# Performance work log

Hardware: AMD Instinct MI355X
Metric: run time of the kernel (lower is better)

Reference implementation:

```python
import jax, jax.numpy as jnp
import numpy as np

B, H, S, D = 4, 16, 2048, 64


def setup_inputs() -> dict:
    key = jax.random.key(0)
    kq, kk, kv, kp = jax.random.split(key, 4)
    query = jax.random.normal(kq, (B, H, S, D), dtype=jnp.float32)
    k = jax.random.normal(kk, (B, H, S, D), dtype=jnp.float32)
    value = jax.random.normal(kv, (B, H, S, D), dtype=jnp.float32)
    # 0/1 key-padding mask, broadcastable against the [S, S] causal mask
    padding_mask = jax.random.randint(kp, (B, 1, 1, S), 0, 2, dtype=jnp.int32)
    return {"query": query, "key": k, "value": value, "padding_mask": padding_mask}


def reference(query, key, value, padding_mask):
    d_k = query.shape[-1]
    seq_len = query.shape[-2]
    # scores: [B, H, S, S]
    scores = jnp.einsum("bhqd,bhkd->bhqk", query, key) / jnp.sqrt(jnp.float32(d_k))
    # causal mask: 1 above diagonal
    future = jnp.triu(jnp.ones((seq_len, seq_len), dtype=jnp.float32), k=1)
    combined = future + padding_mask.astype(jnp.float32)  # values in {0,1,2}
    # faithful to torch masked_fill(combined_mask == 1, -1e9): only exact 1 is masked
    scores = jnp.where(combined == 1.0, jnp.float32(-1e9), scores)
    attention_weights = jax.nn.softmax(scores, axis=-1)
    result = attention_weights @ value  # [B, H, S, D]
    return result, attention_weights
```

## Files before the change

### kernel.cpp

```cpp
#include <hip/hip_runtime.h>

#define SEQ 2048
#define DH  64
#define NH  16
#define NB  4
#define NHEADS (NB * NH)
#define NKT 32
#define QT  32
#define NQT (SEQ / QT)
#define NBLK (NHEADS * NQT)
#define KTILE_SH 8192
#define QTILE_SH 4096

typedef _Float16 f16x8 __attribute__((ext_vector_type(8)));
typedef _Float16 f16x4 __attribute__((ext_vector_type(4)));
typedef short    s16x8 __attribute__((ext_vector_type(8)));
typedef float    f32x4 __attribute__((ext_vector_type(4)));

#define MF32(a,b,c) __builtin_amdgcn_mfma_f32_16x16x32_f16(a,b,c,0,0,0)
#define MF16(a,b,c) __builtin_amdgcn_mfma_f32_16x16x16f16(a,b,c,0,0,0)

static __device__ __forceinline__ short f16b(float x) {
    _Float16 h = (_Float16)x;
    return __builtin_bit_cast(short, h);
}

__global__ __launch_bounds__(256) void prep(
    const float* __restrict__ Q, const float* __restrict__ K,
    const float* __restrict__ V, const int* __restrict__ pad,
    short* __restrict__ qimg, short* __restrict__ kimg,
    short* __restrict__ vimg, unsigned* __restrict__ pm)
{
    const int t    = threadIdx.x;
    const int kt   = blockIdx.x & (NKT - 1);
    const int head = blockIdx.x >> 5;
    const size_t rowbase = ((size_t)head * SEQ + (size_t)kt * 64) * DH;

    {
        const int row = t >> 2;
        const int c0  = (t & 3) * 16;
        const int lj  = row & 15;

        {
            const float4* gp = (const float4*)(K + rowbase + (size_t)row * DH + c0);
            const float4 v0 = gp[0], v1 = gp[1], v2 = gp[2], v3 = gp[3];
            const float x[16] = {v0.x,v0.y,v0.z,v0.w, v1.x,v1.y,v1.z,v1.w,
                                 v2.x,v2.y,v2.z,v2.w, v3.x,v3.y,v3.z,v3.w};
            short* tb = kimg + ((size_t)head * NKT + kt) * KTILE_SH + (row >> 4) * 2048;
#pragma unroll
            for (int cg = 0; cg < 2; ++cg) {
                const int col0 = c0 + cg * 8;
                const int dh = col0 >> 5, lg = (col0 & 31) >> 3;
                s16x8 hi8, lo8;
#pragma unroll
                for (int j = 0; j < 8; ++j) {
                    const float xv = x[cg * 8 + j];
                    _Float16 h = (_Float16)xv;
                    hi8[j] = __builtin_bit_cast(short, h);
                    lo8[j] = f16b(xv - (float)h);
                }
                *(s16x8*)&tb[dh * 1024 +       (lg * 16 + lj) * 8] = hi8;
                *(s16x8*)&tb[dh * 1024 + 512 + (lg * 16 + lj) * 8] = lo8;
            }
        }
        {
            const float4* gp = (const float4*)(Q + rowbase + (size_t)row * DH + c0);
            const float4 v0 = gp[0], v1 = gp[1], v2 = gp[2], v3 = gp[3];
            const float x[16] = {v0.x,v0.y,v0.z,v0.w, v1.x,v1.y,v1.z,v1.w,
                                 v2.x,v2.y,v2.z,v2.w, v3.x,v3.y,v3.z,v3.w};
            const int qtile = kt * 2 + (row >> 5);
            const int m     = (row >> 4) & 1;
            short* tb = qimg + ((size_t)head * NQT + qtile) * QTILE_SH + m * 2048;
#pragma unroll
            for (int cg = 0; cg < 2; ++cg) {
                const int col0 = c0 + cg * 8;
                const int dh = col0 >> 5, lg = (col0 & 31) >> 3;
                s16x8 hi8, lo8;
#pragma unroll
                for (int j = 0; j < 8; ++j) {
                    const float xv = x[cg * 8 + j];
                    _Float16 h = (_Float16)xv;
                    hi8[j] = __builtin_bit_cast(short, h);
                    lo8[j] = f16b(xv - (float)h);
                }
                *(s16x8*)&tb[dh * 1024 +       (lg * 16 + lj) * 8] = hi8;
                *(s16x8*)&tb[dh * 1024 + 512 + (lg * 16 + lj) * 8] = lo8;
            }
        }
    }
    {
        const int kc = t >> 6, l = t & 63;
        const int lg = l >> 4, lj = l & 15;
        short* tb = vimg + ((size_t)head * NKT + kt) * KTILE_SH + kc * 2048;
#pragma unroll
        for (int dt = 0; dt < 4; ++dt) {
            s16x8 o;
#pragma unroll
            for (int j = 0; j < 4; ++j) {
                const float xv = V[rowbase + (size_t)(kc * 16 + lg * 4 + j) * DH + dt * 16 + lj];
                _Float16 h = (_Float16)xv;
                o[j]     = __builtin_bit_cast(short, h);
                o[4 + j] = f16b(xv - (float)h);
            }
            *(s16x8*)&tb[dt * 512 + l * 8] = o;
        }
    }
    if (blockIdx.x == 0) {
        const int b = t >> 6, klc = t & 63;
        unsigned mword = 0;
#pragma unroll
        for (int kt2 = 0; kt2 < NKT; ++kt2)
            mword |= (unsigned)(pad[b * SEQ + kt2 * 64 + klc] & 1) << kt2;
        pm[t] = mword;
    }
}

struct KF { f16x8 h0, l0, h1, l1; };

#define LDKF(dst_, kt_) do {                                                   \
    const short* p_ = kb + (size_t)(kt_) * KTILE_SH;                           \
    dst_.h0 = *(const f16x8*)(p_ +        l * 8);                              \
    dst_.l0 = *(const f16x8*)(p_ +  512 + l * 8);                              \
    dst_.h1 = *(const f16x8*)(p_ + 1024 + l * 8);                              \
    dst_.l1 = *(const f16x8*)(p_ + 1536 + l * 8);                              \
} while (0)

#define QK12(kf_, a0_, a1_) do {                                               \
    a0_ = MF32(kf_.h0, qh[0][0], a0_);  a1_ = MF32(kf_.h0, qh[1][0], a1_);     \
    a0_ = MF32(kf_.h0, ql[0][0], a0_);  a1_ = MF32(kf_.h0, ql[1][0], a1_);     \
    a0_ = MF32(kf_.l0, qh[0][0], a0_);  a1_ = MF32(kf_.l0, qh[1][0], a1_);     \
    a0_ = MF32(kf_.h1, qh[0][1], a0_);  a1_ = MF32(kf_.h1, qh[1][1], a1_);     \
    a0_ = MF32(kf_.h1, ql[0][1], a0_);  a1_ = MF32(kf_.h1, ql[1][1], a1_);     \
    a0_ = MF32(kf_.l1, qh[0][1], a0_);  a1_ = MF32(kf_.l1, qh[1][1], a1_);     \
} while (0)

#define P1BODY(kt_, kf_) do {                                                  \
    const short* vp_ = vb + (size_t)(kt_) * KTILE_SH;                          \
    f16x8 vfs_[4];                                                             \
    _Pragma("unroll") for (int dt = 0; dt < 4; ++dt)                           \
        vfs_[dt] = *(const f16x8*)(vp_ + dt * 512 + l * 8);                    \
    f32x4 a0_ = (f32x4){0.f,0.f,0.f,0.f}, a1_ = (f32x4){0.f,0.f,0.f,0.f};      \
    QK12(kf_, a0_, a1_);                                                       \
    const int kab_ = (kt_) * 64 + wk * 16 + lg * 4;                            \
    f16x4 w16_[2];                                                             \
    _Pragma("unroll") for (int m = 0; m < 2; ++m) {                            \
        const f32x4 av_ = m ? a1_ : a0_;                                       \
        const int qg_ = qglob + m * 16;                                        \
        float e_[4];                                                           \
        _Pragma("unroll") for (int r = 0; r < 4; ++r) {                        \
            const int ka_ = kab_ + r;                                          \
            const int pd_ = (int)((pmq[r] >> (kt_)) & 1u);                     \
            const bool msk_ = ((ka_ > qg_) != (pd_ == 1));                     \
            e_[r] = __expf((msk_ ? -8.0e9f : av_[r]) * 0.125f);                \
        }                                                                      \
        rs[m] += (e_[0] + e_[1]) + (e_[2] + e_[3]);                            \
        w16_[m] = (f16x4){(_Float16)e_[0], (_Float16)e_[1],                    \
                          (_Float16)e_[2], (_Float16)e_[3]};                   \
    }                                                                          \
    _Pragma("unroll") for (int dt = 0; dt < 4; ++dt) {                         \
        const f16x4 vh_ = __builtin_shufflevector(vfs_[dt], vfs_[dt], 0,1,2,3);\
        const f16x4 vl_ = __builtin_shufflevector(vfs_[dt], vfs_[dt], 4,5,6,7);\
        ov[0][dt] = MF16(w16_[0], vh_, ov[0][dt]);                             \
        ov[1][dt] = MF16(w16_[1], vh_, ov[1][dt]);                             \
        ov[0][dt] = MF16(w16_[0], vl_, ov[0][dt]);                             \
        ov[1][dt] = MF16(w16_[1], vl_, ov[1][dt]);                             \
    }                                                                          \
} while (0)

#define P2BODY(kt_, kf_) do {                                                  \
    f32x4 a0_ = (f32x4){0.f,0.f,0.f,0.f}, a1_ = (f32x4){0.f,0.f,0.f,0.f};      \
    QK12(kf_, a0_, a1_);                                                       \
    const int kab_ = (kt_) * 64 + wk * 16 + lg * 4;                            \
    _Pragma("unroll") for (int m = 0; m < 2; ++m) {                            \
        const f32x4 av_ = m ? a1_ : a0_;                                       \
        const int qg_ = qglob + m * 16;                                        \
        float e_[4];                                                           \
        _Pragma("unroll") for (int r = 0; r < 4; ++r) {                        \
            const int ka_ = kab_ + r;                                          \
            const int pd_ = (int)((pmq[r] >> (kt_)) & 1u);                     \
            const bool msk_ = ((ka_ > qg_) != (pd_ == 1));                     \
            e_[r] = __expf((msk_ ? -8.0e9f : av_[r]) * 0.125f);                \
        }                                                                      \
        f32x4 w4_;                                                             \
        w4_[0] = e_[0] * invr[m]; w4_[1] = e_[1] * invr[m];                    \
        w4_[2] = e_[2] * invr[m]; w4_[3] = e_[3] * invr[m];                    \
        __builtin_nontemporal_store(w4_, (f32x4*)&out_w[wbm[m] + kab_]);       \
    }                                                                          \
} while (0)

__global__ __launch_bounds__(256, 3) void attn_fwd(
    const short* __restrict__ QI, const short* __restrict__ KI,
    const short* __restrict__ VI, const unsigned* __restrict__ PM,
    float* __restrict__ out_res, float* __restrict__ out_w)
{
    __shared__ float s_op[4][QT][65];
    __shared__ float s_red[QT][4];

    const int t = threadIdx.x;
    int bid = blockIdx.x;
    bid = (bid & 7) * (NBLK / 8) + (bid >> 3);

    const int qtile = bid & (NQT - 1);
    const int head  = bid >> 6;
    const int q0    = qtile * QT;
    const size_t hoff = (size_t)head * SEQ * DH;
    const size_t woff = (size_t)head * SEQ * SEQ;

    const int l  = t & 63;
    const int wk = t >> 6;
    const int lj = l & 15;
    const int lg = l >> 4;
    const int qglob = q0 + lj;

    const short* kb  = KI + (size_t)head * NKT * KTILE_SH + wk * 2048;
    const short* vb  = VI + (size_t)head * NKT * KTILE_SH + wk * 2048;
    const short* qbp = QI + ((size_t)head * NQT + qtile) * QTILE_SH;

    f16x8 qh[2][2], ql[2][2];
#pragma unroll
    for (int m = 0; m < 2; ++m)
#pragma unroll
        for (int dh = 0; dh < 2; ++dh) {
            qh[m][dh] = *(const f16x8*)(qbp + m * 2048 + dh * 1024 +       l * 8);
            ql[m][dh] = *(const f16x8*)(qbp + m * 2048 + dh * 1024 + 512 + l * 8);
        }

    int pmq[4];
#pragma unroll
    for (int r = 0; r < 4; ++r)
        pmq[r] = PM[(head >> 4) * 64 + wk * 16 + lg * 4 + r];

    float rs[2] = {0.f, 0.f};
    f32x4 ov[2][4];
#pragma unroll
    for (int m = 0; m < 2; ++m)
#pragma unroll
        for (int dt = 0; dt < 4; ++dt) ov[m][dt] = (f32x4){0.f,0.f,0.f,0.f};

    KF kfA, kfB;
    LDKF(kfA, 0);
#pragma unroll 1
    for (int it = 0; it < NKT / 2; ++it) {
        const int kt0 = it * 2, kt1 = kt0 + 1;
        LDKF(kfB, kt1);
        P1BODY(kt0, kfA);
        LDKF(kfA, (kt1 + 1) & (NKT - 1));
        P1BODY(kt1, kfB);
    }

#pragma unroll
    for (int m = 0; m < 2; ++m) {
        float v = rs[m];
        v += __shfl_xor(v, 16, 64);
        v += __shfl_xor(v, 32, 64);
        rs[m] = v;
    }
    if (lg == 0) {
        s_red[lj][wk]      = rs[0];
        s_red[16 + lj][wk] = rs[1];
    }
#pragma unroll
    for (int m = 0; m < 2; ++m)
#pragma unroll
        for (int dt = 0; dt < 4; ++dt)
#pragma unroll
            for (int r = 0; r < 4; ++r)
                s_op[wk][m * 16 + lg * 4 + r][dt * 16 + lj] = ov[m][dt][r];
    __syncthreads();

    {
        const int q  = t >> 3;
        const int c0 = (t & 7) * 8;
        const float inv = 1.0f / (s_red[q][0] + s_red[q][1] + s_red[q][2] + s_red[q][3]);
        float4 o0, o1;
        o0.x = (s_op[0][q][c0+0]+s_op[1][q][c0+0]+s_op[2][q][c0+0]+s_op[3][q][c0+0]) * inv;
        o0.y = (s_op[0][q][c0+1]+s_op[1][q][c0+1]+s_op[2][q][c0+1]+s_op[3][q][c0+1]) * inv;
        o0.z = (s_op[0][q][c0+2]+s_op[1][q][c0+2]+s_op[2][q][c0+2]+s_op[3][q][c0+2]) * inv;
        o0.w = (s_op[0][q][c0+3]+s_op[1][q][c0+3]+s_op[2][q][c0+3]+s_op[3][q][c0+3]) * inv;
        o1.x = (s_op[0][q][c0+4]+s_op[1][q][c0+4]+s_op[2][q][c0+4]+s_op[3][q][c0+4]) * inv;
        o1.y = (s_op[0][q][c0+5]+s_op[1][q][c0+5]+s_op[2][q][c0+5]+s_op[3][q][c0+5]) * inv;
        o1.z = (s_op[0][q][c0+6]+s_op[1][q][c0+6]+s_op[2][q][c0+6]+s_op[3][q][c0+6]) * inv;
        o1.w = (s_op[0][q][c0+7]+s_op[1][q][c0+7]+s_op[2][q][c0+7]+s_op[3][q][c0+7]) * inv;
        float* op = out_res + hoff + (size_t)(q0 + q) * DH + c0;
        *(float4*)op       = o0;
        *(float4*)(op + 4) = o1;
    }

    float invr[2];
    invr[0] = 1.0f / (s_red[lj][0]      + s_red[lj][1]      + s_red[lj][2]      + s_red[lj][3]);
    invr[1] = 1.0f / (s_red[16 + lj][0] + s_red[16 + lj][1] + s_red[16 + lj][2] + s_red[16 + lj][3]);
    size_t wbm[2];
    wbm[0] = woff + (size_t)(q0 + lj) * SEQ;
    wbm[1] = woff + (size_t)(q0 + 16 + lj) * SEQ;

    LDKF(kfA, 0);
#pragma unroll 1
    for (int it = 0; it < NKT / 2; ++it) {
        const int kt0 = it * 2, kt1 = kt0 + 1;
        LDKF(kfB, kt1);
        P2BODY(kt0, kfA);
        LDKF(kfA, (kt1 + 1) & (NKT - 1));
        P2BODY(kt1, kfB);
    }
}

extern "C" void kernel_launch(void* const* d_in, const int* in_sizes, int n_in,
                              void* d_out, int out_size, void* d_ws, size_t ws_size,
                              hipStream_t stream) {
    const float* Q   = (const float*)d_in[0];
    const float* K   = (const float*)d_in[1];
    const float* V   = (const float*)d_in[2];
    const int*   pad = (const int*)d_in[3];
    float* out_res = (float*)d_out;
    float* out_w   = out_res + (size_t)NB * NH * SEQ * DH;

    short* qimg = (short*)d_ws;
    short* kimg = qimg + (size_t)NHEADS * NQT * QTILE_SH;
    short* vimg = kimg + (size_t)NHEADS * NKT * KTILE_SH;
    unsigned* pm = (unsigned*)(vimg + (size_t)NHEADS * NKT * KTILE_SH);

    prep<<<dim3(NHEADS * NKT), 256, 0, stream>>>(Q, K, V, pad, qimg, kimg, vimg, pm);
    attn_fwd<<<dim3(NBLK), 256, 0, stream>>>(qimg, kimg, vimg, pm, out_res, out_w);
}
```

Baseline: 1.362 ms.

## Double query tile per block to 64 rows and prefetch V fragments

Each block now covers 64 query rows instead of 32. Every K/V fragment loaded from global/L2 is therefore reused across four 16-row MFMA groups instead of two, which halves the K and V traffic per query. V fragments are also double-buffered alongside K so their loads overlap the previous tile's compute. The cost is higher register use (more Q fragments and accumulators), so launch bounds drop to 2 blocks per CU and occupancy may fall.

```diff
diff --git a/kernel.cpp b/kernel.cpp
--- a/kernel.cpp
+++ b/kernel.cpp
@@ -6,11 +6,11 @@
 #define NB  4
 #define NHEADS (NB * NH)
 #define NKT 32
-#define QT  32
+#define QT  64
 #define NQT (SEQ / QT)
 #define NBLK (NHEADS * NQT)
 #define KTILE_SH 8192
-#define QTILE_SH 4096
+#define QTILE_SH 8192
 
 typedef _Float16 f16x8 __attribute__((ext_vector_type(8)));
 typedef _Float16 f16x4 __attribute__((ext_vector_type(4)));
@@ -68,9 +68,8 @@
             const float4 v0 = gp[0], v1 = gp[1], v2 = gp[2], v3 = gp[3];
             const float x[16] = {v0.x,v0.y,v0.z,v0.w, v1.x,v1.y,v1.z,v1.w,
                                  v2.x,v2.y,v2.z,v2.w, v3.x,v3.y,v3.z,v3.w};
-            const int qtile = kt * 2 + (row >> 5);
-            const int m     = (row >> 4) & 1;
-            short* tb = qimg + ((size_t)head * NQT + qtile) * QTILE_SH + m * 2048;
+            const int m = row >> 4;
+            short* tb = qimg + ((size_t)head * NQT + kt) * QTILE_SH + m * 2048;
 #pragma unroll
             for (int cg = 0; cg < 2; ++cg) {
                 const int col0 = c0 + cg * 8;
@@ -116,6 +115,7 @@
 }
 
 struct KF { f16x8 h0, l0, h1, l1; };
+struct VF { f16x8 v0, v1, v2, v3; };
 
 #define LDKF(dst_, kt_) do {                                                   \
     const short* p_ = kb + (size_t)(kt_) * KTILE_SH;                           \
@@ -125,26 +125,37 @@
     dst_.l1 = *(const f16x8*)(p_ + 1536 + l * 8);                              \
 } while (0)
 
-#define QK12(kf_, a0_, a1_) do {                                               \
+#define LDVF(dst_, kt_) do {                                                   \
+    const short* p_ = vb + (size_t)(kt_) * KTILE_SH;                           \
+    dst_.v0 = *(const f16x8*)(p_ +        l * 8);                              \
+    dst_.v1 = *(const f16x8*)(p_ +  512 + l * 8);                              \
+    dst_.v2 = *(const f16x8*)(p_ + 1024 + l * 8);                              \
+    dst_.v3 = *(const f16x8*)(p_ + 1536 + l * 8);                              \
+} while (0)
+
+#define QK24(kf_, a0_, a1_, a2_, a3_) do {                                     \
     a0_ = MF32(kf_.h0, qh[0][0], a0_);  a1_ = MF32(kf_.h0, qh[1][0], a1_);     \
+    a2_ = MF32(kf_.h0, qh[2][0], a2_);  a3_ = MF32(kf_.h0, qh[3][0], a3_);     \
     a0_ = MF32(kf_.h0, ql[0][0], a0_);  a1_ = MF32(kf_.h0, ql[1][0], a1_);     \
+    a2_ = MF32(kf_.h0, ql[2][0], a2_);  a3_ = MF32(kf_.h0, ql[3][0], a3_);     \
     a0_ = MF32(kf_.l0, qh[0][0], a0_);  a1_ = MF32(kf_.l0, qh[1][0], a1_);     \
+    a2_ = MF32(kf_.l0, qh[2][0], a2_);  a3_ = MF32(kf_.l0, qh[3][0], a3_);     \
     a0_ = MF32(kf_.h1, qh[0][1], a0_);  a1_ = MF32(kf_.h1, qh[1][1], a1_);     \
+    a2_ = MF32(kf_.h1, qh[2][1], a2_);  a3_ = MF32(kf_.h1, qh[3][1], a3_);     \
     a0_ = MF32(kf_.h1, ql[0][1], a0_);  a1_ = MF32(kf_.h1, ql[1][1], a1_);     \
+    a2_ = MF32(kf_.h1, ql[2][1], a2_);  a3_ = MF32(kf_.h1, ql[3][1], a3_);     \
     a0_ = MF32(kf_.l1, qh[0][1], a0_);  a1_ = MF32(kf_.l1, qh[1][1], a1_);     \
-} while (0)
-
-#define P1BODY(kt_, kf_) do {                                                  \
-    const short* vp_ = vb + (size_t)(kt_) * KTILE_SH;                          \
-    f16x8 vfs_[4];                                                             \
-    _Pragma("unroll") for (int dt = 0; dt < 4; ++dt)                           \
-        vfs_[dt] = *(const f16x8*)(vp_ + dt * 512 + l * 8);                    \
+    a2_ = MF32(kf_.l1, qh[2][1], a2_);  a3_ = MF32(kf_.l1, qh[3][1], a3_);     \
+} while (0)
+
+#define P1BODY(kt_, kf_, vf_) do {                                             \
     f32x4 a0_ = (f32x4){0.f,0.f,0.f,0.f}, a1_ = (f32x4){0.f,0.f,0.f,0.f};      \
-    QK12(kf_, a0_, a1_);                                                       \
+    f32x4 a2_ = (f32x4){0.f,0.f,0.f,0.f}, a3_ = (f32x4){0.f,0.f,0.f,0.f};      \
+    QK24(kf_, a0_, a1_, a2_, a3_);                                             \
     const int kab_ = (kt_) * 64 + wk * 16 + lg * 4;                            \
-    f16x4 w16_[2];                                                             \
-    _Pragma("unroll") for (int m = 0; m < 2; ++m) {                            \
-        const f32x4 av_ = m ? a1_ : a0_;                                       \
+    f16x4 w16_[4];                                                             \
+    _Pragma("unroll") for (int m = 0; m < 4; ++m) {                            \
+        const f32x4 av_ = (m==0) ? a0_ : (m==1) ? a1_ : (m==2) ? a2_ : a3_;    \
         const int qg_ = qglob + m * 16;                                        \
         float e_[4];                                                           \
         _Pragma("unroll") for (int r = 0; r < 4; ++r) {                        \
@@ -158,21 +169,28 @@
                           (_Float16)e_[2], (_Float16)e_[3]};                   \
     }                                                                          \
     _Pragma("unroll") for (int dt = 0; dt < 4; ++dt) {                         \
-        const f16x4 vh_ = __builtin_shufflevector(vfs_[dt], vfs_[dt], 0,1,2,3);\
-        const f16x4 vl_ = __builtin_shufflevector(vfs_[dt], vfs_[dt], 4,5,6,7);\
+        const f16x8 vv_ = (dt==0) ? vf_.v0 : (dt==1) ? vf_.v1                  \
+                        : (dt==2) ? vf_.v2 : vf_.v3;                           \
+        const f16x4 vh_ = __builtin_shufflevector(vv_, vv_, 0,1,2,3);          \
+        const f16x4 vl_ = __builtin_shufflevector(vv_, vv_, 4,5,6,7);          \
         ov[0][dt] = MF16(w16_[0], vh_, ov[0][dt]);                             \
         ov[1][dt] = MF16(w16_[1], vh_, ov[1][dt]);                             \
+        ov[2][dt] = MF16(w16_[2], vh_, ov[2][dt]);                             \
+        ov[3][dt] = MF16(w16_[3], vh_, ov[3][dt]);                             \
         ov[0][dt] = MF16(w16_[0], vl_, ov[0][dt]);                             \
         ov[1][dt] = MF16(w16_[1], vl_, ov[1][dt]);                             \
+        ov[2][dt] = MF16(w16_[2], vl_, ov[2][dt]);                             \
+        ov[3][dt] = MF16(w16_[3], vl_, ov[3][dt]);                             \
     }                                                                          \
 } while (0)
 
 #define P2BODY(kt_, kf_) do {                                                  \
     f32x4 a0_ = (f32x4){0.f,0.f,0.f,0.f}, a1_ = (f32x4){0.f,0.f,0.f,0.f};      \
-    QK12(kf_, a0_, a1_);                                                       \
+    f32x4 a2_ = (f32x4){0.f,0.f,0.f,0.f}, a3_ = (f32x4){0.f,0.f,0.f,0.f};      \
+    QK24(kf_, a0_, a1_, a2_, a3_);                                             \
     const int kab_ = (kt_) * 64 + wk * 16 + lg * 4;                            \
-    _Pragma("unroll") for (int m = 0; m < 2; ++m) {                            \
-        const f32x4 av_ = m ? a1_ : a0_;                                       \
+    _Pragma("unroll") for (int m = 0; m < 4; ++m) {                            \
+        const f32x4 av_ = (m==0) ? a0_ : (m==1) ? a1_ : (m==2) ? a2_ : a3_;    \
         const int qg_ = qglob + m * 16;                                        \
         float e_[4];                                                           \
         _Pragma("unroll") for (int r = 0; r < 4; ++r) {                        \
@@ -188,7 +206,7 @@
     }                                                                          \
 } while (0)
 
-__global__ __launch_bounds__(256, 3) void attn_fwd(
+__global__ __launch_bounds__(256, 2) void attn_fwd(
     const short* __restrict__ QI, const short* __restrict__ KI,
     const short* __restrict__ VI, const unsigned* __restrict__ PM,
     float* __restrict__ out_res, float* __restrict__ out_w)
@@ -201,7 +219,7 @@
     bid = (bid & 7) * (NBLK / 8) + (bid >> 3);
 
     const int qtile = bid & (NQT - 1);
-    const int head  = bid >> 6;
+    const int head  = bid >> 5;
     const int q0    = qtile * QT;
     const size_t hoff = (size_t)head * SEQ * DH;
     const size_t woff = (size_t)head * SEQ * SEQ;
@@ -216,9 +234,9 @@
     const short* vb  = VI + (size_t)head * NKT * KTILE_SH + wk * 2048;
     const short* qbp = QI + ((size_t)head * NQT + qtile) * QTILE_SH;
 
-    f16x8 qh[2][2], ql[2][2];
-#pragma unroll
-    for (int m = 0; m < 2; ++m)
+    f16x8 qh[4][2], ql[4][2];
+#pragma unroll
+    for (int m = 0; m < 4; ++m)
 #pragma unroll
         for (int dh = 0; dh < 2; ++dh) {
             qh[m][dh] = *(const f16x8*)(qbp + m * 2048 + dh * 1024 +       l * 8);
@@ -230,37 +248,42 @@
     for (int r = 0; r < 4; ++r)
         pmq[r] = PM[(head >> 4) * 64 + wk * 16 + lg * 4 + r];
 
-    float rs[2] = {0.f, 0.f};
-    f32x4 ov[2][4];
-#pragma unroll
-    for (int m = 0; m < 2; ++m)
+    float rs[4] = {0.f, 0.f, 0.f, 0.f};
+    f32x4 ov[4][4];
+#pragma unroll
+    for (int m = 0; m < 4; ++m)
 #pragma unroll
         for (int dt = 0; dt < 4; ++dt) ov[m][dt] = (f32x4){0.f,0.f,0.f,0.f};
 
     KF kfA, kfB;
+    VF vfA, vfB;
     LDKF(kfA, 0);
+    LDVF(vfA, 0);
 #pragma unroll 1
     for (int it = 0; it < NKT / 2; ++it) {
         const int kt0 = it * 2, kt1 = kt0 + 1;
         LDKF(kfB, kt1);
-        P1BODY(kt0, kfA);
+        LDVF(vfB, kt1);
+        P1BODY(kt0, kfA, vfA);
         LDKF(kfA, (kt1 + 1) & (NKT - 1));
-        P1BODY(kt1, kfB);
-    }
-
-#pragma unroll
-    for (int m = 0; m < 2; ++m) {
+        LDVF(vfA, (kt1 + 1) & (NKT - 1));
+        P1BODY(kt1, kfB, vfB);
+    }
+
+#pragma unroll
+    for (int m = 0; m < 4; ++m) {
         float v = rs[m];
         v += __shfl_xor(v, 16, 64);
         v += __shfl_xor(v, 32, 64);
         rs[m] = v;
     }
     if (lg == 0) {
-        s_red[lj][wk]      = rs[0];
-        s_red[16 + lj][wk] = rs[1];
-    }
-#pragma unroll
-    for (int m = 0; m < 2; ++m)
+#pragma unroll
+        for (int m = 0; m < 4; ++m)
+            s_red[m * 16 + lj][wk] = rs[m];
+    }
+#pragma unroll
+    for (int m = 0; m < 4; ++m)
 #pragma unroll
         for (int dt = 0; dt < 4; ++dt)
 #pragma unroll
@@ -269,29 +292,29 @@
     __syncthreads();
 
     {
-        const int q  = t >> 3;
-        const int c0 = (t & 7) * 8;
+        const int q  = t >> 2;
+        const int c0 = (t & 3) * 16;
         const float inv = 1.0f / (s_red[q][0] + s_red[q][1] + s_red[q][2] + s_red[q][3]);
-        float4 o0, o1;
-        o0.x = (s_op[0][q][c0+0]+s_op[1][q][c0+0]+s_op[2][q][c0+0]+s_op[3][q][c0+0]) * inv;
-        o0.y = (s_op[0][q][c0+1]+s_op[1][q][c0+1]+s_op[2][q][c0+1]+s_op[3][q][c0+1]) * inv;
-        o0.z = (s_op[0][q][c0+2]+s_op[1][q][c0+2]+s_op[2][q][c0+2]+s_op[3][q][c0+2]) * inv;
-        o0.w = (s_op[0][q][c0+3]+s_op[1][q][c0+3]+s_op[2][q][c0+3]+s_op[3][q][c0+3]) * inv;
-        o1.x = (s_op[0][q][c0+4]+s_op[1][q][c0+4]+s_op[2][q][c0+4]+s_op[3][q][c0+4]) * inv;
-        o1.y = (s_op[0][q][c0+5]+s_op[1][q][c0+5]+s_op[2][q][c0+5]+s_op[3][q][c0+5]) * inv;
-        o1.z = (s_op[0][q][c0+6]+s_op[1][q][c0+6]+s_op[2][q][c0+6]+s_op[3][q][c0+6]) * inv;
-        o1.w = (s_op[0][q][c0+7]+s_op[1][q][c0+7]+s_op[2][q][c0+7]+s_op[3][q][c0+7]) * inv;
         float* op = out_res + hoff + (size_t)(q0 + q) * DH + c0;
-        *(float4*)op       = o0;
-        *(float4*)(op + 4) = o1;
-    }
-
-    float invr[2];
-    invr[0] = 1.0f / (s_red[lj][0]      + s_red[lj][1]      + s_red[lj][2]      + s_red[lj][3]);
-    invr[1] = 1.0f / (s_red[16 + lj][0] + s_red[16 + lj][1] + s_red[16 + lj][2] + s_red[16 + lj][3]);
-    size_t wbm[2];
-    wbm[0] = woff + (size_t)(q0 + lj) * SEQ;
-    wbm[1] = woff + (size_t)(q0 + 16 + lj) * SEQ;
+#pragma unroll
+        for (int g = 0; g < 4; ++g) {
+            float4 o;
+            o.x = (s_op[0][q][c0+g*4+0]+s_op[1][q][c0+g*4+0]+s_op[2][q][c0+g*4+0]+s_op[3][q][c0+g*4+0]) * inv;
+            o.y = (s_op[0][q][c0+g*4+1]+s_op[1][q][c0+g*4+1]+s_op[2][q][c0+g*4+1]+s_op[3][q][c0+g*4+1]) * inv;
+            o.z = (s_op[0][q][c0+g*4+2]+s_op[1][q][c0+g*4+2]+s_op[2][q][c0+g*4+2]+s_op[3][q][c0+g*4+2]) * inv;
+            o.w = (s_op[0][q][c0+g*4+3]+s_op[1][q][c0+g*4+3]+s_op[2][q][c0+g*4+3]+s_op[3][q][c0+g*4+3]) * inv;
+            *(float4*)(op + g * 4) = o;
+        }
+    }
+
+    float invr[4];
+    size_t wbm[4];
+#pragma unroll
+    for (int m = 0; m < 4; ++m) {
+        const int qq = m * 16 + lj;
+        invr[m] = 1.0f / (s_red[qq][0] + s_red[qq][1] + s_red[qq][2] + s_red[qq][3]);
+        wbm[m]  = woff + (size_t)(q0 + qq) * SEQ;
+    }
 
     LDKF(kfA, 0);
 #pragma unroll 1
```

Result: faster. 1.280 ms (-6.0%).
